# Kernel tuning notes

Measured on AMD Instinct MI355X. Metric: run time of the kernel, lower is better.

Reference implementation:

```python
import math
import jax, jax.numpy as jnp
import numpy as np

B, H, S, D = 2, 16, 2048, 64


def setup_inputs() -> dict:
    key = jax.random.key(0)
    kq, kk, kv = jax.random.split(key, 3)
    query = jax.random.normal(kq, (B, H, S, D), dtype=jnp.float32)
    k = jax.random.normal(kk, (B, H, S, D), dtype=jnp.float32)
    value = jax.random.normal(kv, (B, H, S, D), dtype=jnp.float32)
    # causal mask: True = keep, broadcasts over batch and heads
    mask = jnp.tril(jnp.ones((S, S), dtype=bool))
    return {"query": query, "key": k, "value": value, "mask": mask}


def reference(query, key, value, mask):
    d_k = query.shape[-1]
    scale = 1.0 / math.sqrt(d_k)
    # (..., s1, s2) materialized scores, as in the original module
    scores = jnp.einsum("bhqd,bhkd->bhqk", query, key) * scale
    scores = jnp.where(mask, scores, -jnp.inf)
    # stable softmax = exp(x - max) / sum, same math as the torch softmax helper
    attn = jax.nn.softmax(scores, axis=-1)
    return jnp.einsum("bhqk,bhkd->bhqd", attn, value)
```

## Files before the change

kernel.cpp:

```cpp
#include <hip/hip_runtime.h>
#include <hip/hip_bf16.h>


typedef __attribute__((ext_vector_type(8))) short  s8v;
typedef __attribute__((ext_vector_type(4))) short  s4v;
typedef __attribute__((ext_vector_type(4))) float  f4v;
typedef __attribute__((ext_vector_type(4))) unsigned int u4v;

#define SEQ 2048
#define DH  64
#define BHN 32
#define CSC 0.18033688f

#if __has_builtin(__builtin_amdgcn_exp2f)
#define EXP2(x) __builtin_amdgcn_exp2f(x)
#else
#define EXP2(x) exp2f(x)
#endif

__device__ __forceinline__ unsigned short f2bf(float x) {
  union { float f; unsigned int u; } v; v.f = x;
  return (unsigned short)((v.u + 0x7fffu + ((v.u >> 16) & 1u)) >> 16);
}
__device__ __forceinline__ float bf2f(unsigned short x) {
  union { unsigned int u; float f; } v; v.u = ((unsigned int)x) << 16;
  return v.f;
}
__device__ __forceinline__ int pack_bf2(float a, float b) {
  union { __hip_bfloat162 h; int i; } u;
  u.h = __float22bfloat162_rn(make_float2(a, b));
  return u.i;
}
__device__ __forceinline__ bool probe_is_f32(const unsigned short* p) {
  const unsigned e = (p[threadIdx.x & 63] >> 7) & 0xFFu;
  return __ballot(e >= 0x89u) != 0ULL;
}
__device__ __forceinline__ s8v cvt8(const float* p) {
  float4 a = *(const float4*)p;
  float4 b = *(const float4*)(p + 4);
  s8v r;
  r[0] = (short)f2bf(a.x); r[1] = (short)f2bf(a.y);
  r[2] = (short)f2bf(a.z); r[3] = (short)f2bf(a.w);
  r[4] = (short)f2bf(b.x); r[5] = (short)f2bf(b.y);
  r[6] = (short)f2bf(b.z); r[7] = (short)f2bf(b.w);
  return r;
}
__device__ __forceinline__ s8v cvt8s(const float* p, float s) {
  float4 a = *(const float4*)p;
  float4 b = *(const float4*)(p + 4);
  s8v r;
  r[0] = (short)f2bf(a.x * s); r[1] = (short)f2bf(a.y * s);
  r[2] = (short)f2bf(a.z * s); r[3] = (short)f2bf(a.w * s);
  r[4] = (short)f2bf(b.x * s); r[5] = (short)f2bf(b.y * s);
  r[6] = (short)f2bf(b.z * s); r[7] = (short)f2bf(b.w * s);
  return r;
}

__global__ __launch_bounds__(256) void prep_kernel(
    const void* __restrict__ Kv, const void* __restrict__ Vv,
    unsigned short* __restrict__ Kbf, unsigned short* __restrict__ Vt) {
  const int bh = blockIdx.y;
  const int s0 = blockIdx.x * 64;
  const int t  = threadIdx.x;
  if (blockIdx.z == 0) {
    const unsigned short* K16 = (const unsigned short*)Kv;
    const float*          KF  = (const float*)Kv;
    const bool isF32 = probe_is_f32(K16);
    const int sr = t >> 2, c0 = (t & 3) * 16;
    const size_t base = ((size_t)(bh * SEQ + s0 + sr)) * DH + c0;
    s8v a0, a1;
    if (!isF32) { a0 = *(const s8v*)(K16 + base); a1 = *(const s8v*)(K16 + base + 8); }
    else        { a0 = cvt8(KF + base);           a1 = cvt8(KF + base + 8); }
    *(s8v*)(Kbf + base)     = a0;
    *(s8v*)(Kbf + base + 8) = a1;
  } else {
    __shared__ __align__(16) unsigned short T[64][72];
    const unsigned short* V16 = (const unsigned short*)Vv;
    const float*          VF  = (const float*)Vv;
    const bool isF32 = probe_is_f32(V16);
    {
      const int sr = t >> 2, c0 = (t & 3) * 16;
      const size_t base = ((size_t)(bh * SEQ + s0 + sr)) * DH + c0;
      s8v a0, a1;
      if (!isF32) { a0 = *(const s8v*)(V16 + base); a1 = *(const s8v*)(V16 + base + 8); }
      else        { a0 = cvt8(VF + base);           a1 = cvt8(VF + base + 8); }
      *(s8v*)&T[sr][c0]     = a0;
      *(s8v*)&T[sr][c0 + 8] = a1;
    }
    __syncthreads();
    {
      const int d  = t & 63;
      const int sb = (t >> 6) * 16;
      unsigned int wb[8];
#pragma unroll
      for (int j = 0; j < 8; ++j) {
        unsigned int lo = T[sb + 2 * j][d];
        unsigned int hi = T[sb + 2 * j + 1][d];
        wb[j] = lo | (hi << 16);
      }
      unsigned short* dst = Vt + (size_t)bh * SEQ * DH + (size_t)s0 * 64 + d * 64 + sb;
      u4v q0 = { wb[0], wb[1], wb[2], wb[3] };
      u4v q1 = { wb[4], wb[5], wb[6], wb[7] };
      *(u4v*)dst       = q0;
      *(u4v*)(dst + 8) = q1;
    }
  }
}

__global__ __launch_bounds__(256, 4) void attn_kernel(
    const void* __restrict__ Qv, const unsigned short* __restrict__ Kbf,
    const unsigned short* __restrict__ Vt, void* __restrict__ Outv) {
  __shared__ __align__(16) unsigned short Ks[2][64][72];
  __shared__ __align__(16) unsigned short Vs[2][64][72];

  const unsigned short* Q16 = (const unsigned short*)Qv;
  const float*          QF  = (const float*)Qv;
  const bool isF32 = probe_is_f32(Q16);

  const int blk = blockIdx.x;
  const int bh  = (blk & 7) * 4 + ((blk >> 3) & 3);
  const int a   = (blk >> 5) & 7;
  const int bsl = blk >> 8;
  const int qb  = (bsl == 0) ? (7 - a) : (bsl == 1) ? (8 + a)
                : (bsl == 2) ? (23 - a) : (24 + a);

  const int tid  = threadIdx.x;
  const int w    = tid >> 6;
  const int lane = tid & 63;
  const int quad = lane >> 4;
  const int c16  = lane & 15;
  const int q0   = qb * 64 + w * 16;

  const size_t bh_off = (size_t)bh * SEQ * DH;
  const unsigned short* Kb = Kbf + bh_off;
  const unsigned short* Vb = Vt  + bh_off;

  s8v aq[2];
#pragma unroll
  for (int kc = 0; kc < 2; ++kc) {
    const size_t idx = bh_off + (size_t)(q0 + c16) * DH + kc * 32 + quad * 8;
    if (isF32) aq[kc] = cvt8s(QF + idx, CSC);
    else {
      s8v aa = *(const s8v*)(Q16 + idx);
#pragma unroll
      for (int t = 0; t < 8; ++t)
        aa[t] = (short)f2bf(bf2f((unsigned short)aa[t]) * CSC);
      aq[kc] = aa;
    }
  }

  f4v o[4];
  float l = 0.f;
#pragma unroll
  for (int i = 0; i < 4; ++i) { f4v z = {0.f, 0.f, 0.f, 0.f}; o[i] = z; }

  const int ntiles = qb + 1;

  const int srow = tid >> 2;
  const int scol = (tid & 3) * 16;
  const unsigned short* Kst = Kb + (size_t)srow * DH + scol;
  const unsigned short* Vst = Vb + (size_t)srow * 64 + scol;

  {
    s8v k0 = *(const s8v*)(Kst), k1 = *(const s8v*)(Kst + 8);
    s8v v0 = *(const s8v*)(Vst), v1 = *(const s8v*)(Vst + 8);
    *(s8v*)&Ks[0][srow][scol]     = k0;
    *(s8v*)&Ks[0][srow][scol + 8] = k1;
    *(s8v*)&Vs[0][srow][scol]     = v0;
    *(s8v*)&Vs[0][srow][scol + 8] = v1;
  }
  __syncthreads();

  for (int kt = 0; kt < ntiles; ++kt) {
    const int cb = kt & 1, nb = cb ^ 1;
    const size_t koff = (size_t)((kt + 1 < ntiles) ? kt + 1 : 0) * (64 * DH);
    s8v nk0 = *(const s8v*)(Kst + koff), nk1 = *(const s8v*)(Kst + koff + 8);
    s8v nv0 = *(const s8v*)(Vst + koff), nv1 = *(const s8v*)(Vst + koff + 8);

    s8v kb[4][2];
#pragma unroll
    for (int nt = 0; nt < 4; ++nt) {
      kb[nt][0] = *(const s8v*)&Ks[cb][nt * 16 + c16][quad * 8];
      kb[nt][1] = *(const s8v*)&Ks[cb][nt * 16 + c16][32 + quad * 8];
    }
    s8v vb[4][2];
#pragma unroll
    for (int dt = 0; dt < 4; ++dt)
#pragma unroll
      for (int kc = 0; kc < 2; ++kc) {
        const unsigned short* vr = &Vs[cb][dt * 16 + c16][kc * 32 + quad * 4];
        union { s4v h[2]; s8v v; } uv;
        uv.h[0] = *(const s4v*)(vr);
        uv.h[1] = *(const s4v*)(vr + 16);
        vb[dt][kc] = uv.v;
      }

    float p[4][4];
#pragma unroll
    for (int nt = 0; nt < 4; ++nt) {
      f4v acc = {0.f, 0.f, 0.f, 0.f};
      acc = __builtin_amdgcn_mfma_f32_16x16x32_bf16(kb[nt][0], aq[0], acc, 0, 0, 0);
      acc = __builtin_amdgcn_mfma_f32_16x16x32_bf16(kb[nt][1], aq[1], acc, 0, 0, 0);
#pragma unroll
      for (int r = 0; r < 4; ++r) p[nt][r] = EXP2(acc[r]);
    }
    if (kt * 64 + 63 > q0) {
      const int qmk = q0 + c16 - kt * 64 - quad * 4;
#pragma unroll
      for (int nt = 0; nt < 4; ++nt)
#pragma unroll
        for (int r = 0; r < 4; ++r)
          if (nt * 16 + r > qmk) p[nt][r] = 0.f;
    }
    float s = 0.f;
#pragma unroll
    for (int nt = 0; nt < 4; ++nt)
      s += (p[nt][0] + p[nt][1]) + (p[nt][2] + p[nt][3]);
    l += s;
#pragma unroll
    for (int kc = 0; kc < 2; ++kc) {
      union { int d[4]; s8v v; } u;
      u.d[0] = pack_bf2(p[2 * kc][0],     p[2 * kc][1]);
      u.d[1] = pack_bf2(p[2 * kc][2],     p[2 * kc][3]);
      u.d[2] = pack_bf2(p[2 * kc + 1][0], p[2 * kc + 1][1]);
      u.d[3] = pack_bf2(p[2 * kc + 1][2], p[2 * kc + 1][3]);
#pragma unroll
      for (int dt = 0; dt < 4; ++dt)
        o[dt] = __builtin_amdgcn_mfma_f32_16x16x32_bf16(u.v, vb[dt][kc], o[dt], 0, 0, 0);
    }

    *(s8v*)&Ks[nb][srow][scol]     = nk0;
    *(s8v*)&Ks[nb][srow][scol + 8] = nk1;
    *(s8v*)&Vs[nb][srow][scol]     = nv0;
    *(s8v*)&Vs[nb][srow][scol + 8] = nv1;
    __syncthreads();
  }

  {
    float lv = l;
    lv += __shfl_xor(lv, 16);
    lv += __shfl_xor(lv, 32);
    union { float f; int i; } lu; lu.f = lv;
    float invr[4];
#pragma unroll
    for (int rr = 0; rr < 4; ++rr) {
      union { int i; float f; } tf;
      tf.i = __builtin_amdgcn_ds_bpermute(4 * (quad * 4 + rr), lu.i);
      invr[rr] = 1.0f / tf.f;
    }
    if (isF32) {
      float* OF = (float*)Outv;
#pragma unroll
      for (int rr = 0; rr < 4; ++rr) {
        const size_t rb = bh_off + (size_t)(q0 + quad * 4 + rr) * DH + c16;
#pragma unroll
        for (int dt = 0; dt < 4; ++dt)
          OF[rb + dt * 16] = o[dt][rr] * invr[rr];
      }
    } else {
      unsigned short* O16 = (unsigned short*)Outv;
#pragma unroll
      for (int rr = 0; rr < 4; ++rr) {
        const size_t rb = bh_off + (size_t)(q0 + quad * 4 + rr) * DH + c16;
#pragma unroll
        for (int dt = 0; dt < 4; ++dt)
          O16[rb + dt * 16] = f2bf(o[dt][rr] * invr[rr]);
      }
    }
  }
}

extern "C" void kernel_launch(void* const* d_in, const int* in_sizes, int n_in,
                              void* d_out, int out_size, void* d_ws, size_t ws_size,
                              hipStream_t stream) {
  const void* Q = d_in[0];
  const void* K = d_in[1];
  const void* V = d_in[2];
  unsigned short* Kbf = (unsigned short*)d_ws;
  unsigned short* Vt  = Kbf + (size_t)BHN * SEQ * DH;

  dim3 g1(SEQ / 64, BHN, 2);
  prep_kernel<<<g1, 256, 0, stream>>>(K, V, Kbf, Vt);
  attn_kernel<<<dim3(1024), 256, 0, stream>>>(Q, Kbf, Vt, d_out);
}
```

Baseline: 142.8 us.

## Give each wave two 16-row query subtiles and pre-permute V layout

Each workgroup shrinks to 128 threads (2 waves). Each wave now processes 32 query rows as two 16-row halves, so the K and V fragments loaded from shared memory are reused across both halves. The prep kernel writes V transposed in an interleaved order that matches the MFMA operand layout, which lets the attention kernel load V fragments with one 16-byte LDS read instead of two 8-byte reads. The cost is more registers per wave (two output accumulators, two probability tiles) and fewer waves per workgroup to hide latency. Launch bounds also change.

Measured after the change: 140.2 us. About the same (-1.9%).

```diff
diff --git a/kernel.cpp b/kernel.cpp
--- a/kernel.cpp
+++ b/kernel.cpp
@@ -3,7 +3,6 @@
 
 
 typedef __attribute__((ext_vector_type(8))) short  s8v;
-typedef __attribute__((ext_vector_type(4))) short  s4v;
 typedef __attribute__((ext_vector_type(4))) float  f4v;
 typedef __attribute__((ext_vector_type(4))) unsigned int u4v;
 
@@ -90,24 +89,26 @@
     __syncthreads();
     {
       const int d  = t & 63;
-      const int sb = (t >> 6) * 16;
-      unsigned int wb[8];
-#pragma unroll
-      for (int j = 0; j < 8; ++j) {
-        unsigned int lo = T[sb + 2 * j][d];
-        unsigned int hi = T[sb + 2 * j + 1][d];
-        wb[j] = lo | (hi << 16);
-      }
-      unsigned short* dst = Vt + (size_t)bh * SEQ * DH + (size_t)s0 * 64 + d * 64 + sb;
-      u4v q0 = { wb[0], wb[1], wb[2], wb[3] };
-      u4v q1 = { wb[4], wb[5], wb[6], wb[7] };
-      *(u4v*)dst       = q0;
-      *(u4v*)(dst + 8) = q1;
+      const int hs = t >> 6;
+      unsigned short* dst = Vt + (size_t)bh * SEQ * DH + (size_t)s0 * 64
+                          + (size_t)d * 64 + hs * 16;
+#pragma unroll
+      for (int cc = 0; cc < 2; ++cc) {
+        const int c  = hs * 2 + cc;
+        const int kA = (c >> 2) * 32 + (c & 3) * 4;
+        unsigned int wb[4];
+        wb[0] = (unsigned int)T[kA + 0][d]  | ((unsigned int)T[kA + 1][d]  << 16);
+        wb[1] = (unsigned int)T[kA + 2][d]  | ((unsigned int)T[kA + 3][d]  << 16);
+        wb[2] = (unsigned int)T[kA + 16][d] | ((unsigned int)T[kA + 17][d] << 16);
+        wb[3] = (unsigned int)T[kA + 18][d] | ((unsigned int)T[kA + 19][d] << 16);
+        u4v q = { wb[0], wb[1], wb[2], wb[3] };
+        *(u4v*)(dst + cc * 8) = q;
+      }
     }
   }
 }
 
-__global__ __launch_bounds__(256, 4) void attn_kernel(
+__global__ __launch_bounds__(128, 2) void attn_kernel(
     const void* __restrict__ Qv, const unsigned short* __restrict__ Kbf,
     const unsigned short* __restrict__ Vt, void* __restrict__ Outv) {
   __shared__ __align__(16) unsigned short Ks[2][64][72];
@@ -129,53 +130,66 @@
   const int lane = tid & 63;
   const int quad = lane >> 4;
   const int c16  = lane & 15;
-  const int q0   = qb * 64 + w * 16;
+  const int q0   = qb * 64 + w * 32;
 
   const size_t bh_off = (size_t)bh * SEQ * DH;
   const unsigned short* Kb = Kbf + bh_off;
   const unsigned short* Vb = Vt  + bh_off;
 
-  s8v aq[2];
-#pragma unroll
-  for (int kc = 0; kc < 2; ++kc) {
-    const size_t idx = bh_off + (size_t)(q0 + c16) * DH + kc * 32 + quad * 8;
-    if (isF32) aq[kc] = cvt8s(QF + idx, CSC);
-    else {
-      s8v aa = *(const s8v*)(Q16 + idx);
-#pragma unroll
-      for (int t = 0; t < 8; ++t)
-        aa[t] = (short)f2bf(bf2f((unsigned short)aa[t]) * CSC);
-      aq[kc] = aa;
-    }
-  }
-
-  f4v o[4];
-  float l = 0.f;
-#pragma unroll
-  for (int i = 0; i < 4; ++i) { f4v z = {0.f, 0.f, 0.f, 0.f}; o[i] = z; }
+  s8v aq[2][2];
+#pragma unroll
+  for (int h = 0; h < 2; ++h)
+#pragma unroll
+    for (int kc = 0; kc < 2; ++kc) {
+      const size_t idx = bh_off + (size_t)(q0 + h * 16 + c16) * DH + kc * 32 + quad * 8;
+      if (isF32) aq[h][kc] = cvt8s(QF + idx, CSC);
+      else {
+        s8v aa = *(const s8v*)(Q16 + idx);
+#pragma unroll
+        for (int t = 0; t < 8; ++t)
+          aa[t] = (short)f2bf(bf2f((unsigned short)aa[t]) * CSC);
+        aq[h][kc] = aa;
+      }
+    }
+
+  f4v o[2][4];
+  float l[2] = {0.f, 0.f};
+#pragma unroll
+  for (int h = 0; h < 2; ++h)
+#pragma unroll
+    for (int i = 0; i < 4; ++i) { f4v z = {0.f, 0.f, 0.f, 0.f}; o[h][i] = z; }
 
   const int ntiles = qb + 1;
 
-  const int srow = tid >> 2;
-  const int scol = (tid & 3) * 16;
+  const int srow = tid >> 1;
+  const int scol = (tid & 1) * 32;
   const unsigned short* Kst = Kb + (size_t)srow * DH + scol;
   const unsigned short* Vst = Vb + (size_t)srow * 64 + scol;
 
   {
-    s8v k0 = *(const s8v*)(Kst), k1 = *(const s8v*)(Kst + 8);
-    s8v v0 = *(const s8v*)(Vst), v1 = *(const s8v*)(Vst + 8);
-    *(s8v*)&Ks[0][srow][scol]     = k0;
-    *(s8v*)&Ks[0][srow][scol + 8] = k1;
-    *(s8v*)&Vs[0][srow][scol]     = v0;
-    *(s8v*)&Vs[0][srow][scol + 8] = v1;
+    s8v k0[4], v0[4];
+#pragma unroll
+    for (int j = 0; j < 4; ++j) {
+      k0[j] = *(const s8v*)(Kst + j * 8);
+      v0[j] = *(const s8v*)(Vst + j * 8);
+    }
+#pragma unroll
+    for (int j = 0; j < 4; ++j) {
+      *(s8v*)&Ks[0][srow][scol + j * 8] = k0[j];
+      *(s8v*)&Vs[0][srow][scol + j * 8] = v0[j];
+    }
   }
   __syncthreads();
 
   for (int kt = 0; kt < ntiles; ++kt) {
     const int cb = kt & 1, nb = cb ^ 1;
     const size_t koff = (size_t)((kt + 1 < ntiles) ? kt + 1 : 0) * (64 * DH);
-    s8v nk0 = *(const s8v*)(Kst + koff), nk1 = *(const s8v*)(Kst + koff + 8);
-    s8v nv0 = *(const s8v*)(Vst + koff), nv1 = *(const s8v*)(Vst + koff + 8);
+    s8v nk[4], nv[4];
+#pragma unroll
+    for (int j = 0; j < 4; ++j) {
+      nk[j] = *(const s8v*)(Kst + koff + j * 8);
+      nv[j] = *(const s8v*)(Vst + koff + j * 8);
+    }
 
     s8v kb[4][2];
 #pragma unroll
@@ -187,57 +201,62 @@
 #pragma unroll
     for (int dt = 0; dt < 4; ++dt)
 #pragma unroll
+      for (int kc = 0; kc < 2; ++kc)
+        vb[dt][kc] = *(const s8v*)&Vs[cb][dt * 16 + c16][(kc * 4 + quad) * 8];
+
+    float p[2][4][4];
+#pragma unroll
+    for (int h = 0; h < 2; ++h)
+#pragma unroll
+      for (int nt = 0; nt < 4; ++nt) {
+        f4v acc = {0.f, 0.f, 0.f, 0.f};
+        acc = __builtin_amdgcn_mfma_f32_16x16x32_bf16(kb[nt][0], aq[h][0], acc, 0, 0, 0);
+        acc = __builtin_amdgcn_mfma_f32_16x16x32_bf16(kb[nt][1], aq[h][1], acc, 0, 0, 0);
+#pragma unroll
+        for (int r = 0; r < 4; ++r) p[h][nt][r] = EXP2(acc[r]);
+      }
+    if (kt * 64 + 63 > q0) {
+#pragma unroll
+      for (int h = 0; h < 2; ++h) {
+        const int qmk = q0 + h * 16 + c16 - kt * 64 - quad * 4;
+#pragma unroll
+        for (int nt = 0; nt < 4; ++nt)
+#pragma unroll
+          for (int r = 0; r < 4; ++r)
+            if (nt * 16 + r > qmk) p[h][nt][r] = 0.f;
+      }
+    }
+#pragma unroll
+    for (int h = 0; h < 2; ++h) {
+      float s = 0.f;
+#pragma unroll
+      for (int nt = 0; nt < 4; ++nt)
+        s += (p[h][nt][0] + p[h][nt][1]) + (p[h][nt][2] + p[h][nt][3]);
+      l[h] += s;
+#pragma unroll
       for (int kc = 0; kc < 2; ++kc) {
-        const unsigned short* vr = &Vs[cb][dt * 16 + c16][kc * 32 + quad * 4];
-        union { s4v h[2]; s8v v; } uv;
-        uv.h[0] = *(const s4v*)(vr);
-        uv.h[1] = *(const s4v*)(vr + 16);
-        vb[dt][kc] = uv.v;
-      }
-
-    float p[4][4];
-#pragma unroll
-    for (int nt = 0; nt < 4; ++nt) {
-      f4v acc = {0.f, 0.f, 0.f, 0.f};
-      acc = __builtin_amdgcn_mfma_f32_16x16x32_bf16(kb[nt][0], aq[0], acc, 0, 0, 0);
-      acc = __builtin_amdgcn_mfma_f32_16x16x32_bf16(kb[nt][1], aq[1], acc, 0, 0, 0);
-#pragma unroll
-      for (int r = 0; r < 4; ++r) p[nt][r] = EXP2(acc[r]);
-    }
-    if (kt * 64 + 63 > q0) {
-      const int qmk = q0 + c16 - kt * 64 - quad * 4;
-#pragma unroll
-      for (int nt = 0; nt < 4; ++nt)
-#pragma unroll
-        for (int r = 0; r < 4; ++r)
-          if (nt * 16 + r > qmk) p[nt][r] = 0.f;
-    }
-    float s = 0.f;
-#pragma unroll
-    for (int nt = 0; nt < 4; ++nt)
-      s += (p[nt][0] + p[nt][1]) + (p[nt][2] + p[nt][3]);
-    l += s;
-#pragma unroll
-    for (int kc = 0; kc < 2; ++kc) {
-      union { int d[4]; s8v v; } u;
-      u.d[0] = pack_bf2(p[2 * kc][0],     p[2 * kc][1]);
-      u.d[1] = pack_bf2(p[2 * kc][2],     p[2 * kc][3]);
-      u.d[2] = pack_bf2(p[2 * kc + 1][0], p[2 * kc + 1][1]);
-      u.d[3] = pack_bf2(p[2 * kc + 1][2], p[2 * kc + 1][3]);
-#pragma unroll
-      for (int dt = 0; dt < 4; ++dt)
-        o[dt] = __builtin_amdgcn_mfma_f32_16x16x32_bf16(u.v, vb[dt][kc], o[dt], 0, 0, 0);
-    }
-
-    *(s8v*)&Ks[nb][srow][scol]     = nk0;
-    *(s8v*)&Ks[nb][srow][scol + 8] = nk1;
-    *(s8v*)&Vs[nb][srow][scol]     = nv0;
-    *(s8v*)&Vs[nb][srow][scol + 8] = nv1;
+        union { int d[4]; s8v v; } u;
+        u.d[0] = pack_bf2(p[h][2 * kc][0],     p[h][2 * kc][1]);
+        u.d[1] = pack_bf2(p[h][2 * kc][2],     p[h][2 * kc][3]);
+        u.d[2] = pack_bf2(p[h][2 * kc + 1][0], p[h][2 * kc + 1][1]);
+        u.d[3] = pack_bf2(p[h][2 * kc + 1][2], p[h][2 * kc + 1][3]);
+#pragma unroll
+        for (int dt = 0; dt < 4; ++dt)
+          o[h][dt] = __builtin_amdgcn_mfma_f32_16x16x32_bf16(u.v, vb[dt][kc], o[h][dt], 0, 0, 0);
+      }
+    }
+
+#pragma unroll
+    for (int j = 0; j < 4; ++j) {
+      *(s8v*)&Ks[nb][srow][scol + j * 8] = nk[j];
+      *(s8v*)&Vs[nb][srow][scol + j * 8] = nv[j];
+    }
     __syncthreads();
   }
 
-  {
-    float lv = l;
+#pragma unroll
+  for (int h = 0; h < 2; ++h) {
+    float lv = l[h];
     lv += __shfl_xor(lv, 16);
     lv += __shfl_xor(lv, 32);
     union { float f; int i; } lu; lu.f = lv;
@@ -252,19 +271,19 @@
       float* OF = (float*)Outv;
 #pragma unroll
       for (int rr = 0; rr < 4; ++rr) {
-        const size_t rb = bh_off + (size_t)(q0 + quad * 4 + rr) * DH + c16;
+        const size_t rb = bh_off + (size_t)(q0 + h * 16 + quad * 4 + rr) * DH + c16;
 #pragma unroll
         for (int dt = 0; dt < 4; ++dt)
-          OF[rb + dt * 16] = o[dt][rr] * invr[rr];
+          OF[rb + dt * 16] = o[h][dt][rr] * invr[rr];
       }
     } else {
       unsigned short* O16 = (unsigned short*)Outv;
 #pragma unroll
       for (int rr = 0; rr < 4; ++rr) {
-        const size_t rb = bh_off + (size_t)(q0 + quad * 4 + rr) * DH + c16;
+        const size_t rb = bh_off + (size_t)(q0 + h * 16 + quad * 4 + rr) * DH + c16;
 #pragma unroll
         for (int dt = 0; dt < 4; ++dt)
-          O16[rb + dt * 16] = f2bf(o[dt][rr] * invr[rr]);
+          O16[rb + dt * 16] = f2bf(o[h][dt][rr] * invr[rr]);
       }
     }
   }
@@ -281,5 +300,5 @@
 
   dim3 g1(SEQ / 64, BHN, 2);
   prep_kernel<<<g1, 256, 0, stream>>>(K, V, Kbf, Vt);
-  attn_kernel<<<dim3(1024), 256, 0, stream>>>(Q, Kbf, Vt, d_out);
-}
+  attn_kernel<<<dim3(1024), 128, 0, stream>>>(Q, Kbf, Vt, d_out);
+}
```
